# Kernel optimization log

Measured on AMD Instinct MI355X. Metric: run time of the kernel, lower is better.

## Reference

```python
import jax, jax.numpy as jnp
import numpy as np

B, S, D, H, L = 8, 512, 1024, 16, 2
DH = D // H
EPS = 1e-6
SCALE = float(np.sqrt(DH))


def _ln(x, g, b):
    # custom LayerNormalization: unbiased std (torch default), eps added to std
    m = x.mean(axis=-1, keepdims=True)
    s = jnp.std(x, axis=-1, keepdims=True, ddof=1)
    return g * (x - m) / (s + EPS) + b


def _pos_encoding(seq_len, dim):
    pos = jnp.arange(seq_len, dtype=jnp.float32)[:, None]
    dims = jnp.arange(dim, dtype=jnp.float32)
    div = 10000.0 ** (2.0 * dims / dim)
    pe = jnp.zeros((seq_len, dim), jnp.float32)
    pe = pe.at[:, 0::2].set(jnp.sin(pos / div[0::2]))
    pe = pe.at[:, 1::2].set(jnp.cos(pos / div[1::2]))
    return pe


def setup_inputs() -> dict:
    key = jax.random.key(0)
    ks = jax.random.split(key, 20)
    std = 0.02
    p = lambda k, shape: jax.random.normal(k, shape, jnp.float32) * std
    return {
        "features": jax.random.normal(ks[0], (B, S, D), jnp.float32),
        "mask": jnp.ones((B, S), jnp.int32),
        "ln_in_g": jnp.ones((D,), jnp.float32),
        "ln_in_b": jnp.zeros((D,), jnp.float32),
        "Wq": p(ks[1], (L, D, D)), "bq": p(ks[2], (L, D)),
        "Wk": p(ks[3], (L, D, D)), "bk": p(ks[4], (L, D)),
        "Wv": p(ks[5], (L, D, D)), "bv": p(ks[6], (L, D)),
        "Wo": p(ks[7], (L, D, D)), "bo": p(ks[8], (L, D)),
        "ln1_g": jnp.ones((L, D), jnp.float32), "ln1_b": jnp.zeros((L, D), jnp.float32),
        "W1": p(ks[9], (L, D, D)), "b1": p(ks[10], (L, D)),
        "W2": p(ks[11], (L, D, D)), "b2": p(ks[12], (L, D)),
        "ln2_g": jnp.ones((L, D), jnp.float32), "ln2_b": jnp.zeros((L, D), jnp.float32),
    }


def reference(features, mask, ln_in_g, ln_in_b, Wq, bq, Wk, bk, Wv, bv, Wo, bo,
              ln1_g, ln1_b, W1, b1, W2, b2, ln2_g, ln2_b):
    # input norm + positional encoding (dropout inert at eval)
    x = _ln(features, ln_in_g, ln_in_b) + _pos_encoding(S, D)  # [B,S,D]
    # mask: positions where mask==0 are masked out with -1e18
    neg = (mask == 0)[:, None, None, :]  # [B,1,1,Sk]

    def encoder_layer(inp, i):
        q = (inp @ Wq[i].T + bq[i]).reshape(B, S, H, DH).transpose(0, 2, 1, 3)
        k = (inp @ Wk[i].T + bk[i]).reshape(B, S, H, DH).transpose(0, 2, 1, 3)
        v = (inp @ Wv[i].T + bv[i]).reshape(B, S, H, DH).transpose(0, 2, 1, 3)
        scores = jnp.einsum('bhqd,bhkd->bhqk', q, k) / SCALE
        scores = jnp.where(neg, -1e18, scores)
        attn = jax.nn.softmax(scores, axis=-1)
        ctx = jnp.einsum('bhqk,bhkd->bhqd', attn, v).transpose(0, 2, 1, 3).reshape(B, S, D)
        attn_out = ctx @ Wo[i].T + bo[i]
        s = _ln(attn_out + inp, ln1_g[i], ln1_b[i])  # residual + custom LN
        h = jax.nn.gelu(s @ W1[i].T + b1[i], approximate=False)
        f = h @ W2[i].T + b2[i]
        return _ln(f + s, ln2_g[i], ln2_b[i])

    # FAITHFUL to source: layers are NOT chained -- each layer reads the
    # original (query,key,value); output is the last layer's result.
    out = x
    for i in range(L):
        out = encoder_layer(x, i)
    return out
```

## Files before the change

### kernel.cpp

```cpp
#include <hip/hip_runtime.h>
#include <cstdint>
#include <cstddef>


typedef __attribute__((ext_vector_type(8))) short bf16x8;
typedef __attribute__((ext_vector_type(4))) short bf16x4;
typedef __attribute__((ext_vector_type(4))) float f32x4;

#define MFMA16(a, b, c) __builtin_amdgcn_mfma_f32_16x16x32_bf16((a), (b), (c), 0, 0, 0)

__device__ __forceinline__ unsigned short f2b(float f) {
  union { float f; unsigned int u; } x; x.f = f;
  unsigned int r = x.u + 0x7fffu + ((x.u >> 16) & 1u);
  return (unsigned short)(r >> 16);
}

__device__ __forceinline__ void gl_lds16(const void* g, void* l) {
  __builtin_amdgcn_global_load_lds(
      (const __attribute__((address_space(1))) void*)g,
      (__attribute__((address_space(3))) void*)l, 16, 0, 0);
}

template <int BN, int EPI>
__global__ __launch_bounds__(256) void gemm_t(
    const unsigned short* __restrict__ A, const unsigned short* __restrict__ B,
    const float* __restrict__ bias, float* __restrict__ outF,
    unsigned short* __restrict__ outB, int N, int K, int nnHalf) {
  __shared__ char la[2 * 128 * 128];
  __shared__ char lb[2 * BN * 128];
  constexpr int NR = BN / 32;
  const int tid = threadIdx.x;
  const int l = tid & 63, w = tid >> 6;
  const int l15 = l & 15, l4 = l >> 4;
  const int xcd = blockIdx.x & 7, r = blockIdx.x >> 3;
  const int m0 = ((xcd >> 1) * 8 + (r & 7)) * 128;
  const int n0 = ((xcd & 1) * nnHalf + (r >> 3)) * BN;
  const int wr = (w >> 1) * 64, wc = (w & 1) * (BN / 2);
  const int NT = K >> 6;

#define STAGE(buf, t)                                                         \
  {                                                                           \
    const int k0_ = (t) * 64;                                                 \
    _Pragma("unroll") for (int i = 0; i < 4; ++i) {                           \
      const int c = i * 256 + tid;                                            \
      const int row = c >> 3;                                                 \
      const int gch = (c & 7) ^ (row & 7);                                    \
      gl_lds16(A + (size_t)(m0 + row) * K + k0_ + gch * 8,                    \
               la + (buf) * 16384 + (i * 256 + w * 64) * 16);                 \
    }                                                                         \
    _Pragma("unroll") for (int i = 0; i < BN / 32; ++i) {                     \
      const int c = i * 256 + tid;                                            \
      const int row = c >> 3;                                                 \
      const int gch = (c & 7) ^ (row & 7);                                    \
      gl_lds16(B + (size_t)(n0 + row) * K + k0_ + gch * 8,                    \
               lb + (buf) * (BN * 128) + (i * 256 + w * 64) * 16);            \
    }                                                                         \
  }

  f32x4 acc[4][NR] = {};
  const int sw = l15 & 7;

  STAGE(0, 0);
  __syncthreads();

  for (int t = 0; t < NT; ++t) {
    if (t + 1 < NT) {
      STAGE((t + 1) & 1, t + 1);
      __builtin_amdgcn_sched_barrier(0);
    }
    const char* abuf = la + (t & 1) * 16384;
    const char* bbuf = lb + (t & 1) * (BN * 128);
#pragma unroll
    for (int kk = 0; kk < 2; ++kk) {
      const unsigned int ch = (unsigned int)(((kk * 4 + l4) ^ sw) << 4);
      bf16x8 af[4], bfr[NR];
#pragma unroll
      for (int m = 0; m < 4; ++m)
        af[m] = *(const bf16x8*)(abuf + (wr + m * 16 + l15) * 128 + ch);
#pragma unroll
      for (int n = 0; n < NR; ++n)
        bfr[n] = *(const bf16x8*)(bbuf + (wc + n * 16 + l15) * 128 + ch);
#pragma unroll
      for (int m = 0; m < 4; ++m) {
#pragma unroll
        for (int n = 0; n < NR; ++n) {
          acc[m][n] = MFMA16(af[m], bfr[n], acc[m][n]);
        }
      }
    }
    __syncthreads();
  }
#undef STAGE

#pragma unroll
  for (int m = 0; m < 4; ++m) {
#pragma unroll
    for (int n = 0; n < NR; ++n) {
      const int col = n0 + wc + n * 16 + l15;
      const float bb = bias[col];
#pragma unroll
      for (int e = 0; e < 4; ++e) {
        const int row = m0 + wr + m * 16 + l4 * 4 + e;
        float v = acc[m][n][e] + bb;
        if (EPI == 0) {
          outF[(size_t)row * N + col] = v;
        } else if (EPI == 1) {
          if (col < 1024) v *= 0.125f;
          outB[(size_t)row * N + col] = f2b(v);
        } else {
          v = 0.5f * v * (1.f + erff(v * 0.70710678118654752f));
          outB[(size_t)row * N + col] = f2b(v);
        }
      }
    }
  }
}

__global__ __launch_bounds__(256, 2) void attn_kernel(
    const unsigned short* __restrict__ qkv, const int* __restrict__ mask,
    unsigned short* __restrict__ ctx) {
  extern __shared__ char smem[];
  float* maskadd = (float*)(smem + 65536);
  const int bid = blockIdx.x;
  const int b = bid & 7, h = (bid >> 3) & 15, qt = bid >> 7;
  const int tid = threadIdx.x, l = tid & 63, w = tid >> 6;
  const int l15 = l & 15, l4 = l >> 4;
  const size_t RB = (size_t)b * 512 * 3072;

  for (int s = tid; s < 512; s += 256)
    maskadd[s] = mask[b * 512 + s] ? 0.f : -1e18f;

  const unsigned short* Kbase = qkv + RB + 1024 + h * 64;
  const unsigned short* Vbase = qkv + RB + 2048 + h * 64;

  const int kr0 = tid >> 2, kc0 = tid & 3;
  const unsigned int swzk = (unsigned int)((kr0 & 7) << 4);
  const unsigned int ka0 = ((unsigned int)(kr0 * 128 + kc0 * 16)) ^ swzk;
  const unsigned int ka1 = ((unsigned int)(kr0 * 128 + kc0 * 16 + 64)) ^ swzk;
  const int vs0 = 2 * l, vd0 = w * 16;

  bf16x8 k00, k01, k10, k11, vreg[4];
  k00 = *(const bf16x8*)(Kbase + (size_t)kr0 * 3072 + kc0 * 8);
  k01 = *(const bf16x8*)(Kbase + (size_t)kr0 * 3072 + kc0 * 8 + 32);
  k10 = *(const bf16x8*)(Kbase + (size_t)(kr0 + 64) * 3072 + kc0 * 8);
  k11 = *(const bf16x8*)(Kbase + (size_t)(kr0 + 64) * 3072 + kc0 * 8 + 32);
  vreg[0] = *(const bf16x8*)(Vbase + (size_t)vs0 * 3072 + vd0);
  vreg[1] = *(const bf16x8*)(Vbase + (size_t)vs0 * 3072 + vd0 + 8);
  vreg[2] = *(const bf16x8*)(Vbase + (size_t)(vs0 + 1) * 3072 + vd0);
  vreg[3] = *(const bf16x8*)(Vbase + (size_t)(vs0 + 1) * 3072 + vd0 + 8);

  const int q0 = qt * 64 + w * 16;
  const unsigned short* qb =
      qkv + RB + (size_t)(q0 + l15) * 3072 + h * 64 + l4 * 8;
  const bf16x8 qf0 = *(const bf16x8*)(qb);
  const bf16x8 qf1 = *(const bf16x8*)(qb + 32);

#define KWRITE(dst)                        \
  {                                        \
    *(bf16x8*)((dst) + ka0) = k00;         \
    *(bf16x8*)((dst) + ka1) = k01;         \
    *(bf16x8*)((dst) + ka0 + 8192) = k10;  \
    *(bf16x8*)((dst) + ka1 + 8192) = k11;  \
  }
#define VWRITE(dst)                                                          \
  {                                                                          \
    _Pragma("unroll") for (int j = 0; j < 16; ++j) {                         \
      const unsigned short lo_ =                                             \
          (unsigned short)((j < 8) ? vreg[0][j] : vreg[1][j - 8]);           \
      const unsigned short hi_ =                                             \
          (unsigned short)((j < 8) ? vreg[2][j] : vreg[3][j - 8]);           \
      *(unsigned int*)((dst) +                                               \
                       (((vd0 + j) * 256 + vs0 * 2) ^ ((j & 7) << 4))) =     \
          (unsigned int)lo_ | ((unsigned int)hi_ << 16);                     \
    }                                                                        \
  }

  KWRITE(smem);
  VWRITE(smem + 32768);
  __syncthreads();

  const int hi4 = l4 >> 1, gl = l4 & 1, g2 = l4 & 2;
  f32x4 acc[4] = {};
  float run_m = -1e30f, run_s = 0.f;

#pragma unroll
  for (int t = 0; t < 4; ++t) {
    char* kcur = smem + (t & 1) * 16384;
    char* vcur = smem + 32768 + (t & 1) * 16384;
    if (t < 3) {
      const int sn = (t + 1) * 128;
      k00 = *(const bf16x8*)(Kbase + (size_t)(sn + kr0) * 3072 + kc0 * 8);
      k01 = *(const bf16x8*)(Kbase + (size_t)(sn + kr0) * 3072 + kc0 * 8 + 32);
      k10 = *(const bf16x8*)(Kbase + (size_t)(sn + kr0 + 64) * 3072 + kc0 * 8);
      k11 = *(const bf16x8*)(Kbase + (size_t)(sn + kr0 + 64) * 3072 + kc0 * 8 + 32);
      vreg[0] = *(const bf16x8*)(Vbase + (size_t)(sn + vs0) * 3072 + vd0);
      vreg[1] = *(const bf16x8*)(Vbase + (size_t)(sn + vs0) * 3072 + vd0 + 8);
      vreg[2] = *(const bf16x8*)(Vbase + (size_t)(sn + vs0 + 1) * 3072 + vd0);
      vreg[3] = *(const bf16x8*)(Vbase + (size_t)(sn + vs0 + 1) * 3072 + vd0 + 8);
      __builtin_amdgcn_sched_barrier(0);
    }
    f32x4 sc[8];
    __builtin_amdgcn_s_setprio(1);
#pragma unroll
    for (int kk = 0; kk < 8; ++kk) {
      const unsigned int lin = (unsigned int)((kk * 16 + l15) * 128 + l4 * 16);
      const unsigned int swz = (unsigned int)((l15 & 7) << 4);
      const bf16x8 af0 = *(const bf16x8*)(kcur + (lin ^ swz));
      const bf16x8 af1 = *(const bf16x8*)(kcur + ((lin + 64) ^ swz));
      f32x4 c = {0.f, 0.f, 0.f, 0.f};
      c = MFMA16(af0, qf0, c);
      c = MFMA16(af1, qf1, c);
      sc[kk] = c;
    }
    __builtin_amdgcn_s_setprio(0);
    float tmx = -1e30f;
#pragma unroll
    for (int kk = 0; kk < 8; ++kk) {
#pragma unroll
      for (int e = 0; e < 4; ++e) {
        const float v = sc[kk][e] + maskadd[t * 128 + kk * 16 + l4 * 4 + e];
        sc[kk][e] = v;
        tmx = fmaxf(tmx, v);
      }
    }
    tmx = fmaxf(tmx, __shfl_xor(tmx, 16));
    tmx = fmaxf(tmx, __shfl_xor(tmx, 32));
    const float nm = (t == 0) ? tmx : fmaxf(run_m, tmx);
    float tsum = 0.f;
    unsigned int pk[8][2];
#pragma unroll
    for (int kk = 0; kk < 8; ++kk) {
      const float p0 = __expf(sc[kk][0] - nm);
      const float p1 = __expf(sc[kk][1] - nm);
      const float p2 = __expf(sc[kk][2] - nm);
      const float p3 = __expf(sc[kk][3] - nm);
      tsum += (p0 + p1) + (p2 + p3);
      asm("v_cvt_pk_bf16_f32 %0, %1, %2" : "=v"(pk[kk][0]) : "v"(p0), "v"(p1));
      asm("v_cvt_pk_bf16_f32 %0, %1, %2" : "=v"(pk[kk][1]) : "v"(p2), "v"(p3));
    }
    tsum += __shfl_xor(tsum, 16);
    tsum += __shfl_xor(tsum, 32);
    if (t == 0) {
      run_s = tsum;
    } else {
      const float scale = __expf(run_m - nm);
      run_s = run_s * scale + tsum;
      float s4[4];
#pragma unroll
      for (int e = 0; e < 4; ++e) s4[e] = __shfl(scale, l4 * 4 + e);
#pragma unroll
      for (int nt = 0; nt < 4; ++nt) {
#pragma unroll
        for (int e = 0; e < 4; ++e) acc[nt][e] *= s4[e];
      }
    }
    run_m = nm;
#pragma unroll
    for (int k2 = 0; k2 < 4; ++k2) {
      const unsigned int own0 = hi4 ? pk[2 * k2 + 1][0] : pk[2 * k2][0];
      const unsigned int own1 = hi4 ? pk[2 * k2 + 1][1] : pk[2 * k2][1];
      const unsigned int oth0 = hi4 ? pk[2 * k2][0] : pk[2 * k2 + 1][0];
      const unsigned int oth1 = hi4 ? pk[2 * k2][1] : pk[2 * k2 + 1][1];
      const unsigned int s16_0 = (unsigned int)__shfl_xor((int)own0, 16);
      const unsigned int s16_1 = (unsigned int)__shfl_xor((int)own1, 16);
      const unsigned int s32_0 = (unsigned int)__shfl_xor((int)oth0, 32);
      const unsigned int s32_1 = (unsigned int)__shfl_xor((int)oth1, 32);
      const unsigned int s48_0 = (unsigned int)__shfl_xor((int)oth0, 48);
      const unsigned int s48_1 = (unsigned int)__shfl_xor((int)oth1, 48);
      union { unsigned int u[4]; bf16x8 v; } pa;
      pa.u[0] = g2 ? (gl ? s16_0 : s32_0) : (gl ? s48_0 : own0);
      pa.u[1] = g2 ? (gl ? s16_1 : s32_1) : (gl ? s48_1 : own1);
      pa.u[2] = g2 ? (gl ? own0 : s48_0) : (gl ? s32_0 : s16_0);
      pa.u[3] = g2 ? (gl ? own1 : s48_1) : (gl ? s32_1 : s16_1);
      __builtin_amdgcn_s_setprio(1);
#pragma unroll
      for (int nt = 0; nt < 4; ++nt) {
        const int d = nt * 16 + l15;
        const unsigned int vb =
            (unsigned int)((d * 256 + k2 * 64 + l4 * 16) ^ ((l15 & 7) << 4));
        const bf16x8 vbf = *(const bf16x8*)(vcur + vb);
        acc[nt] = MFMA16(pa.v, vbf, acc[nt]);
      }
      __builtin_amdgcn_s_setprio(0);
    }
    if (t < 3) {
      char* knxt = smem + ((t + 1) & 1) * 16384;
      char* vnxt = smem + 32768 + ((t + 1) & 1) * 16384;
      KWRITE(knxt);
      VWRITE(vnxt);
      __syncthreads();
    }
  }
#undef KWRITE
#undef VWRITE

  const float inv = 1.f / run_s;
  float invq[4];
#pragma unroll
  for (int e = 0; e < 4; ++e) invq[e] = __shfl(inv, l4 * 4 + e);
#pragma unroll
  for (int nt = 0; nt < 4; ++nt) {
#pragma unroll
    for (int e = 0; e < 4; ++e) {
      const size_t row = (size_t)b * 512 + q0 + l4 * 4 + e;
      ctx[row * 1024 + h * 64 + nt * 16 + l15] = f2b(acc[nt][e] * invq[e]);
    }
  }
}

__global__ __launch_bounds__(256) void ln_kernel(
    const float* __restrict__ A, const float* __restrict__ R,
    const float* __restrict__ g, const float* __restrict__ bta,
    float* __restrict__ outF, unsigned short* __restrict__ outB, int addPE) {
  __shared__ float red[8];
  const int row = blockIdx.x, tid = threadIdx.x;
  const size_t base = (size_t)row * 1024 + tid * 4;
  float4 a = *(const float4*)(A + base);
  if (R) {
    const float4 r = *(const float4*)(R + base);
    a.x += r.x; a.y += r.y; a.z += r.z; a.w += r.w;
  }
  float s = a.x + a.y + a.z + a.w;
  float q = a.x * a.x + a.y * a.y + a.z * a.z + a.w * a.w;
#pragma unroll
  for (int o = 32; o; o >>= 1) {
    s += __shfl_xor(s, o);
    q += __shfl_xor(q, o);
  }
  if ((tid & 63) == 0) {
    red[(tid >> 6) * 2] = s;
    red[(tid >> 6) * 2 + 1] = q;
  }
  __syncthreads();
  const float S = red[0] + red[2] + red[4] + red[6];
  const float Qs = red[1] + red[3] + red[5] + red[7];
  const float mean = S * (1.f / 1024.f);
  float var = (Qs - 1024.f * mean * mean) * (1.f / 1023.f);
  var = fmaxf(var, 0.f);
  const float inv = 1.f / (sqrtf(var) + 1e-6f);
  float o4[4] = {a.x, a.y, a.z, a.w};
#pragma unroll
  for (int j = 0; j < 4; ++j) {
    const int col = tid * 4 + j;
    float y = g[col] * (o4[j] - mean) * inv + bta[col];
    if (addPE) {
      const float ang = (float)(row & 511) * exp2f((float)col * -0.025952563241307518f);
      y += (col & 1) ? cosf(ang) : sinf(ang);
    }
    o4[j] = y;
  }
  *(float4*)(outF + base) = make_float4(o4[0], o4[1], o4[2], o4[3]);
  if (outB) {
    bf16x4 pb;
    pb[0] = (short)f2b(o4[0]);
    pb[1] = (short)f2b(o4[1]);
    pb[2] = (short)f2b(o4[2]);
    pb[3] = (short)f2b(o4[3]);
    *(bf16x4*)(outB + base) = pb;
  }
}

__global__ __launch_bounds__(256) void prep_weights(
    const float* __restrict__ Wq, const float* __restrict__ Wk,
    const float* __restrict__ Wv, const float* __restrict__ Wo,
    const float* __restrict__ W1, const float* __restrict__ W2,
    const float* __restrict__ bq, const float* __restrict__ bk,
    const float* __restrict__ bv, unsigned short* __restrict__ wqkv,
    unsigned short* __restrict__ wo, unsigned short* __restrict__ w1,
    unsigned short* __restrict__ w2, float* __restrict__ bqkv) {
  const int gid = blockIdx.x * 256 + threadIdx.x;
  if (gid < 1572864) {
    const int chunk = gid >> 18;
    const int off = (gid & 262143) * 4;
    const float* s;
    unsigned short* d;
    switch (chunk) {
      case 0: s = Wq; d = wqkv; break;
      case 1: s = Wk; d = wqkv + 1048576; break;
      case 2: s = Wv; d = wqkv + 2097152; break;
      case 3: s = Wo; d = wo; break;
      case 4: s = W1; d = w1; break;
      default: s = W2; d = w2; break;
    }
    const float4 v = *(const float4*)(s + off);
    bf16x4 o;
    o[0] = (short)f2b(v.x); o[1] = (short)f2b(v.y);
    o[2] = (short)f2b(v.z); o[3] = (short)f2b(v.w);
    *(bf16x4*)(d + off) = o;
  } else {
    const int idx = (gid - 1572864) * 4;
    if (idx < 3072) {
      const float* bs = idx < 1024 ? bq : (idx < 2048 ? bk - 1024 : bv - 2048);
      *(float4*)(bqkv + idx) = *(const float4*)(bs + idx);
    }
  }
}

extern "C" void kernel_launch(void* const* d_in, const int* in_sizes, int n_in,
                              void* d_out, int out_size, void* d_ws, size_t ws_size,
                              hipStream_t stream) {
  (void)in_sizes; (void)n_in; (void)out_size; (void)ws_size;
  const float* features = (const float*)d_in[0];
  const int* mask = (const int*)d_in[1];
  const float* ln_in_g = (const float*)d_in[2];
  const float* ln_in_b = (const float*)d_in[3];
  const size_t DD = 1024 * 1024;
  const float* Wq = (const float*)d_in[4] + DD;
  const float* bq = (const float*)d_in[5] + 1024;
  const float* Wk = (const float*)d_in[6] + DD;
  const float* bk = (const float*)d_in[7] + 1024;
  const float* Wv = (const float*)d_in[8] + DD;
  const float* bv = (const float*)d_in[9] + 1024;
  const float* Wo = (const float*)d_in[10] + DD;
  const float* bo = (const float*)d_in[11] + 1024;
  const float* l1g = (const float*)d_in[12] + 1024;
  const float* l1b = (const float*)d_in[13] + 1024;
  const float* W1 = (const float*)d_in[14] + DD;
  const float* b1 = (const float*)d_in[15] + 1024;
  const float* W2 = (const float*)d_in[16] + DD;
  const float* b2 = (const float*)d_in[17] + 1024;
  const float* l2g = (const float*)d_in[18] + 1024;
  const float* l2b = (const float*)d_in[19] + 1024;

  char* base = (char*)d_ws;
  float* x_f32 = (float*)(base);
  float* tmp_f32 = (float*)(base + 16777216);
  float* s_f32 = (float*)(base + 33554432);
  unsigned short* qkv = (unsigned short*)(base + 50331648);
  unsigned short* xb = (unsigned short*)(base + 75497472);
  unsigned short* ctxb = (unsigned short*)(base + 83886080);
  unsigned short* wqkv = (unsigned short*)(base + 92274688);
  unsigned short* wo = (unsigned short*)(base + 98566144);
  unsigned short* w1 = (unsigned short*)(base + 100663296);
  unsigned short* w2 = (unsigned short*)(base + 102760448);
  float* bqkv = (float*)(base + 104857600);

  prep_weights<<<6147, 256, 0, stream>>>(Wq, Wk, Wv, Wo, W1, W2, bq, bk, bv,
                                         wqkv, wo, w1, w2, bqkv);
  ln_kernel<<<4096, 256, 0, stream>>>(features, nullptr, ln_in_g, ln_in_b, x_f32, xb, 1);
  gemm_t<128, 1><<<768, 256, 0, stream>>>(xb, wqkv, bqkv, nullptr, qkv, 3072, 1024, 12);
  hipFuncSetAttribute((const void*)attn_kernel,
                      hipFuncAttributeMaxDynamicSharedMemorySize, 67584);
  attn_kernel<<<1024, 256, 67584, stream>>>(qkv, mask, ctxb);
  gemm_t<64, 0><<<512, 256, 0, stream>>>(ctxb, wo, bo, tmp_f32, nullptr, 1024, 1024, 8);
  ln_kernel<<<4096, 256, 0, stream>>>(tmp_f32, x_f32, l1g, l1b, s_f32, ctxb, 0);
  gemm_t<64, 2><<<512, 256, 0, stream>>>(ctxb, w1, b1, nullptr, xb, 1024, 1024, 8);
  gemm_t<64, 0><<<512, 256, 0, stream>>>(xb, w2, b2, tmp_f32, nullptr, 1024, 1024, 8);
  ln_kernel<<<4096, 256, 0, stream>>>(tmp_f32, s_f32, l2g, l2b, (float*)d_out, nullptr, 0);
}
```

Baseline: 179.5 us.

## Triple-buffer GEMM LDS staging with explicit vmcnt waits and single barrier

Switches the bf16 GEMM from double to triple buffering in dynamic LDS, prefetching two K-tiles ahead. Each iteration now ends with a partial s_waitcnt vmcnt and one raw s_barrier, replacing the full __syncthreads. The goal is to hide global-to-LDS load latency behind MFMA work. The cost is more LDS per block (96KB/72KB), which can reduce blocks per CU, and hand-counted vmcnt values that must match the number of loads issued per stage.

```diff
diff --git a/kernel.cpp b/kernel.cpp
--- a/kernel.cpp
+++ b/kernel.cpp
@@ -26,8 +26,9 @@
     const unsigned short* __restrict__ A, const unsigned short* __restrict__ B,
     const float* __restrict__ bias, float* __restrict__ outF,
     unsigned short* __restrict__ outB, int N, int K, int nnHalf) {
-  __shared__ char la[2 * 128 * 128];
-  __shared__ char lb[2 * BN * 128];
+  extern __shared__ char smem[];
+  char* la = smem;
+  char* lb = smem + 3 * 16384;
   constexpr int NR = BN / 32;
   const int tid = threadIdx.x;
   const int l = tid & 63, w = tid >> 6;
@@ -56,20 +57,32 @@
                lb + (buf) * (BN * 128) + (i * 256 + w * 64) * 16);            \
     }                                                                         \
   }
+#define WAIT_L()                                                   \
+  {                                                                \
+    if constexpr (BN == 128) {                                     \
+      asm volatile("s_waitcnt vmcnt(8)" ::: "memory");             \
+    } else {                                                       \
+      asm volatile("s_waitcnt vmcnt(6)" ::: "memory");             \
+    }                                                              \
+  }
 
   f32x4 acc[4][NR] = {};
   const int sw = l15 & 7;
 
   STAGE(0, 0);
-  __syncthreads();
+  STAGE(1, 1);
+  WAIT_L();
+  __builtin_amdgcn_sched_barrier(0);
+  __builtin_amdgcn_s_barrier();
+  __builtin_amdgcn_sched_barrier(0);
 
   for (int t = 0; t < NT; ++t) {
-    if (t + 1 < NT) {
-      STAGE((t + 1) & 1, t + 1);
-      __builtin_amdgcn_sched_barrier(0);
-    }
-    const char* abuf = la + (t & 1) * 16384;
-    const char* bbuf = lb + (t & 1) * (BN * 128);
+    if (t + 2 < NT) {
+      STAGE((t + 2) % 3, t + 2);
+    }
+    __builtin_amdgcn_sched_barrier(0);
+    const char* abuf = la + (t % 3) * 16384;
+    const char* bbuf = lb + (t % 3) * (BN * 128);
 #pragma unroll
     for (int kk = 0; kk < 2; ++kk) {
       const unsigned int ch = (unsigned int)(((kk * 4 + l4) ^ sw) << 4);
@@ -88,9 +101,19 @@
         }
       }
     }
-    __syncthreads();
+    if (t < NT - 1) {
+      if (t + 2 < NT) {
+        WAIT_L();
+      } else {
+        asm volatile("s_waitcnt vmcnt(0)" ::: "memory");
+      }
+      __builtin_amdgcn_sched_barrier(0);
+      __builtin_amdgcn_s_barrier();
+      __builtin_amdgcn_sched_barrier(0);
+    }
   }
 #undef STAGE
+#undef WAIT_L
 
 #pragma unroll
   for (int m = 0; m < 4; ++m) {
@@ -435,16 +458,23 @@
   unsigned short* w2 = (unsigned short*)(base + 102760448);
   float* bqkv = (float*)(base + 104857600);
 
+  hipFuncSetAttribute((const void*)gemm_t<128, 1>,
+                      hipFuncAttributeMaxDynamicSharedMemorySize, 98304);
+  hipFuncSetAttribute((const void*)gemm_t<64, 0>,
+                      hipFuncAttributeMaxDynamicSharedMemorySize, 73728);
+  hipFuncSetAttribute((const void*)gemm_t<64, 2>,
+                      hipFuncAttributeMaxDynamicSharedMemorySize, 73728);
+  hipFuncSetAttribute((const void*)attn_kernel,
+                      hipFuncAttributeMaxDynamicSharedMemorySize, 67584);
+
   prep_weights<<<6147, 256, 0, stream>>>(Wq, Wk, Wv, Wo, W1, W2, bq, bk, bv,
                                          wqkv, wo, w1, w2, bqkv);
   ln_kernel<<<4096, 256, 0, stream>>>(features, nullptr, ln_in_g, ln_in_b, x_f32, xb, 1);
-  gemm_t<128, 1><<<768, 256, 0, stream>>>(xb, wqkv, bqkv, nullptr, qkv, 3072, 1024, 12);
-  hipFuncSetAttribute((const void*)attn_kernel,
-                      hipFuncAttributeMaxDynamicSharedMemorySize, 67584);
+  gemm_t<128, 1><<<768, 256, 98304, stream>>>(xb, wqkv, bqkv, nullptr, qkv, 3072, 1024, 12);
   attn_kernel<<<1024, 256, 67584, stream>>>(qkv, mask, ctxb);
-  gemm_t<64, 0><<<512, 256, 0, stream>>>(ctxb, wo, bo, tmp_f32, nullptr, 1024, 1024, 8);
+  gemm_t<64, 0><<<512, 256, 73728, stream>>>(ctxb, wo, bo, tmp_f32, nullptr, 1024, 1024, 8);
   ln_kernel<<<4096, 256, 0, stream>>>(tmp_f32, x_f32, l1g, l1b, s_f32, ctxb, 0);
-  gemm_t<64, 2><<<512, 256, 0, stream>>>(ctxb, w1, b1, nullptr, xb, 1024, 1024, 8);
-  gemm_t<64, 0><<<512, 256, 0, stream>>>(xb, w2, b2, tmp_f32, nullptr, 1024, 1024, 8);
+  gemm_t<64, 2><<<512, 256, 73728, stream>>>(ctxb, w1, b1, nullptr, xb, 1024, 1024, 8);
+  gemm_t<64, 0><<<512, 256, 73728, stream>>>(xb, w2, b2, tmp_f32, nullptr, 1024, 1024, 8);
   ln_kernel<<<4096, 256, 0, stream>>>(tmp_f32, s_f32, l2g, l2b, (float*)d_out, nullptr, 0);
 }
```

After: 172.9 us. 1.04x faster.

## Switch GEMM to triple-buffered K=32 stages with explicit vmcnt waits

Applied to the files above, without the earlier changes.

The GEMM mainloop moves from a double-buffered K=64 tile with __syncthreads to a three-stage ring of K=32 tiles. Loads are issued two stages ahead, and partial s_waitcnt vmcnt counts let the in-flight stage overlap compute before each raw s_barrier. The LDS swizzle is reworked for 64-byte rows. This aims to hide global-to-LDS latency better, at the cost of more barriers per K and less MFMA work between them. The hipFuncSetAttribute call is also moved ahead of the launches.

```diff
diff --git a/kernel.cpp b/kernel.cpp
--- a/kernel.cpp
+++ b/kernel.cpp
@@ -26,9 +26,10 @@
     const unsigned short* __restrict__ A, const unsigned short* __restrict__ B,
     const float* __restrict__ bias, float* __restrict__ outF,
     unsigned short* __restrict__ outB, int N, int K, int nnHalf) {
-  __shared__ char la[2 * 128 * 128];
-  __shared__ char lb[2 * BN * 128];
+  __shared__ char la[3 * 128 * 64];
+  __shared__ char lb[3 * BN * 64];
   constexpr int NR = BN / 32;
+  constexpr int LPS = 2 + BN / 64;
   const int tid = threadIdx.x;
   const int l = tid & 63, w = tid >> 6;
   const int l15 = l & 15, l4 = l >> 4;
@@ -36,61 +37,82 @@
   const int m0 = ((xcd >> 1) * 8 + (r & 7)) * 128;
   const int n0 = ((xcd & 1) * nnHalf + (r >> 3)) * BN;
   const int wr = (w >> 1) * 64, wc = (w & 1) * (BN / 2);
-  const int NT = K >> 6;
+  const int NT = K >> 5;
 
 #define STAGE(buf, t)                                                         \
   {                                                                           \
-    const int k0_ = (t) * 64;                                                 \
-    _Pragma("unroll") for (int i = 0; i < 4; ++i) {                           \
+    const int k0_ = (t) * 32;                                                 \
+    _Pragma("unroll") for (int i = 0; i < 2; ++i) {                           \
       const int c = i * 256 + tid;                                            \
-      const int row = c >> 3;                                                 \
-      const int gch = (c & 7) ^ (row & 7);                                    \
+      const int row = c >> 2;                                                 \
+      const int gch = (c & 3) ^ (row & 3);                                    \
       gl_lds16(A + (size_t)(m0 + row) * K + k0_ + gch * 8,                    \
-               la + (buf) * 16384 + (i * 256 + w * 64) * 16);                 \
+               la + (buf) * 8192 + c * 16);                                   \
     }                                                                         \
-    _Pragma("unroll") for (int i = 0; i < BN / 32; ++i) {                     \
+    _Pragma("unroll") for (int i = 0; i < BN / 64; ++i) {                     \
       const int c = i * 256 + tid;                                            \
-      const int row = c >> 3;                                                 \
-      const int gch = (c & 7) ^ (row & 7);                                    \
+      const int row = c >> 2;                                                 \
+      const int gch = (c & 3) ^ (row & 3);                                    \
       gl_lds16(B + (size_t)(n0 + row) * K + k0_ + gch * 8,                    \
-               lb + (buf) * (BN * 128) + (i * 256 + w * 64) * 16);            \
+               lb + (buf) * (BN * 64) + c * 16);                              \
     }                                                                         \
   }
+#define WAIT_L()                                                    \
+  {                                                                 \
+    if constexpr (LPS == 4) {                                       \
+      asm volatile("s_waitcnt vmcnt(4)" ::: "memory");              \
+    } else {                                                        \
+      asm volatile("s_waitcnt vmcnt(3)" ::: "memory");              \
+    }                                                               \
+  }
 
   f32x4 acc[4][NR] = {};
-  const int sw = l15 & 7;
+  const unsigned int ch = (unsigned int)((l4 ^ (l15 & 3)) << 4);
 
   STAGE(0, 0);
-  __syncthreads();
-
+  STAGE(1, 1);
+  WAIT_L();
+  __builtin_amdgcn_sched_barrier(0);
+  __builtin_amdgcn_s_barrier();
+  __builtin_amdgcn_sched_barrier(0);
+
+  int cur = 0, stg = 2;
   for (int t = 0; t < NT; ++t) {
-    if (t + 1 < NT) {
-      STAGE((t + 1) & 1, t + 1);
+    if (t + 2 < NT) {
+      STAGE(stg, t + 2);
+    }
+    __builtin_amdgcn_sched_barrier(0);
+    const char* abuf = la + cur * 8192;
+    const char* bbuf = lb + cur * (BN * 64);
+    bf16x8 af[4], bfr[NR];
+#pragma unroll
+    for (int m = 0; m < 4; ++m)
+      af[m] = *(const bf16x8*)(abuf + (wr + m * 16 + l15) * 64 + ch);
+#pragma unroll
+    for (int n = 0; n < NR; ++n)
+      bfr[n] = *(const bf16x8*)(bbuf + (wc + n * 16 + l15) * 64 + ch);
+#pragma unroll
+    for (int m = 0; m < 4; ++m) {
+#pragma unroll
+      for (int n = 0; n < NR; ++n) {
+        acc[m][n] = MFMA16(af[m], bfr[n], acc[m][n]);
+      }
+    }
+    if (t < NT - 1) {
+      if (t + 2 < NT) {
+        WAIT_L();
+      } else {
+        asm volatile("s_waitcnt vmcnt(0)" ::: "memory");
+      }
       __builtin_amdgcn_sched_barrier(0);
-    }
-    const char* abuf = la + (t & 1) * 16384;
-    const char* bbuf = lb + (t & 1) * (BN * 128);
-#pragma unroll
-    for (int kk = 0; kk < 2; ++kk) {
-      const unsigned int ch = (unsigned int)(((kk * 4 + l4) ^ sw) << 4);
-      bf16x8 af[4], bfr[NR];
-#pragma unroll
-      for (int m = 0; m < 4; ++m)
-        af[m] = *(const bf16x8*)(abuf + (wr + m * 16 + l15) * 128 + ch);
-#pragma unroll
-      for (int n = 0; n < NR; ++n)
-        bfr[n] = *(const bf16x8*)(bbuf + (wc + n * 16 + l15) * 128 + ch);
-#pragma unroll
-      for (int m = 0; m < 4; ++m) {
-#pragma unroll
-        for (int n = 0; n < NR; ++n) {
-          acc[m][n] = MFMA16(af[m], bfr[n], acc[m][n]);
-        }
-      }
-    }
-    __syncthreads();
+      __builtin_amdgcn_s_barrier();
+      __builtin_amdgcn_sched_barrier(0);
+    }
+    cur = (cur == 2) ? 0 : cur + 1;
+    stg = (stg == 2) ? 0 : stg + 1;
   }
 #undef STAGE
+#undef WAIT_L
 
 #pragma unroll
   for (int m = 0; m < 4; ++m) {
@@ -435,12 +457,13 @@
   unsigned short* w2 = (unsigned short*)(base + 102760448);
   float* bqkv = (float*)(base + 104857600);
 
+  hipFuncSetAttribute((const void*)attn_kernel,
+                      hipFuncAttributeMaxDynamicSharedMemorySize, 67584);
+
   prep_weights<<<6147, 256, 0, stream>>>(Wq, Wk, Wv, Wo, W1, W2, bq, bk, bv,
                                          wqkv, wo, w1, w2, bqkv);
   ln_kernel<<<4096, 256, 0, stream>>>(features, nullptr, ln_in_g, ln_in_b, x_f32, xb, 1);
   gemm_t<128, 1><<<768, 256, 0, stream>>>(xb, wqkv, bqkv, nullptr, qkv, 3072, 1024, 12);
-  hipFuncSetAttribute((const void*)attn_kernel,
-                      hipFuncAttributeMaxDynamicSharedMemorySize, 67584);
   attn_kernel<<<1024, 256, 67584, stream>>>(qkv, mask, ctxb);
   gemm_t<64, 0><<<512, 256, 0, stream>>>(ctxb, wo, bo, tmp_f32, nullptr, 1024, 1024, 8);
   ln_kernel<<<4096, 256, 0, stream>>>(tmp_f32, x_f32, l1g, l1b, s_f32, ctxb, 0);
```

Result: slower. 185.5 us (+3.4%).
